# Performance work log

Measured on AMD Instinct MI355X. Metric: run time of the kernel, lower is better.

Reference implementation:

```python
import jax, jax.numpy as jnp
import numpy as np

N_EMBEDDING = 512
EMBEDDING_DIM = 64
COMMITMENT_COST = 0.25


def setup_inputs() -> dict:
    key = jax.random.key(0)
    k1, k2 = jax.random.split(key)
    inputs = jax.random.normal(k1, (64, 32, 32, EMBEDDING_DIM), dtype=jnp.float32)
    context = jnp.zeros((1,), dtype=jnp.float32)  # unused by the module
    # variance_scaling(1.0, 'fan_in', 'uniform') on shape (D, K): fan_in = D
    limit = np.sqrt(3.0 / EMBEDDING_DIM)
    embeddings = jax.random.uniform(
        k2, (EMBEDDING_DIM, N_EMBEDDING), dtype=jnp.float32,
        minval=-limit, maxval=limit)
    return {"inputs": inputs, "context": context, "embeddings": embeddings}


def reference(inputs, context, embeddings):
    D, K = embeddings.shape
    flat = inputs.reshape(-1, D)  # [N, D]
    distances = (
        jnp.sum(jnp.square(flat), axis=1, keepdims=True)
        - 2.0 * jnp.matmul(flat, embeddings)
        + jnp.sum(jnp.square(embeddings), axis=0, keepdims=True)
    )
    encoding_indices_flat = jnp.argmax(-distances, axis=1)  # [N]
    encodings = jax.nn.one_hot(encoding_indices_flat, K, dtype=distances.dtype)
    encoding_indices = encoding_indices_flat.reshape(inputs.shape[:-1])
    # gather codebook rows: embeddings.T is [K, D]
    quantized = embeddings.T[encoding_indices]  # [B, H, W, D]

    e_latent_loss = jnp.mean(jnp.square(jax.lax.stop_gradient(quantized) - inputs))
    q_latent_loss = jnp.mean(jnp.square(quantized - jax.lax.stop_gradient(inputs)))
    loss = q_latent_loss + COMMITMENT_COST * e_latent_loss

    # straight-through estimator
    quantized = inputs + jax.lax.stop_gradient(quantized - inputs)

    avg_probs = jnp.mean(encodings, axis=0)
    perplexity = jnp.exp(-jnp.sum(avg_probs * jnp.log(avg_probs + 1e-10)))
    return (quantized, loss, perplexity, encodings, encoding_indices, distances)
```

## Files before the change

### kernel.cpp

```cpp
#include <hip/hip_runtime.h>


#define NROWS 65536
#define DIM 64
#define KCODES 512
#define ROWS_PER_BLOCK 64
#define NBLOCKS (NROWS / ROWS_PER_BLOCK)
#define RPW 8

#define QUANT_OFF 0ull
#define LOSS_OFF  4194304ull
#define PERP_OFF  4194305ull
#define ENC_OFF   4194306ull
#define IDX_OFF   37748738ull
#define DIST_OFF  37814274ull

typedef float f32x4 __attribute__((ext_vector_type(4)));

__global__ __launch_bounds__(64) void vq_transpose(
    const float* __restrict__ emb, float* __restrict__ et)
{
    const int t = blockIdx.x * 64 + threadIdx.x;
    f32x4* et4 = (f32x4*)et;
#pragma unroll
    for (int dq = 0; dq < 16; ++dq) {
        f32x4 v;
        v.x = emb[(dq * 4 + 0) * KCODES + t];
        v.y = emb[(dq * 4 + 1) * KCODES + t];
        v.z = emb[(dq * 4 + 2) * KCODES + t];
        v.w = emb[(dq * 4 + 3) * KCODES + t];
        et4[t * 16 + dq] = v;
    }
}

__global__ __launch_bounds__(512, 2) void vq_main(
    const float* __restrict__ inp, const float* __restrict__ emb,
    const float* __restrict__ et,
    float* __restrict__ out, int* __restrict__ hist,
    float* __restrict__ loss_part)
{
    __shared__ f32x4 s_E[16 * KCODES];
    __shared__ f32x4 s_X[ROWS_PER_BLOCK * 16];
    __shared__ float s_sumx2[ROWS_PER_BLOCK];
    __shared__ float s_loss[8];

    const int tid  = threadIdx.x;
    const int w    = tid >> 6;
    const int lane = tid & 63;
    const int rbase = blockIdx.x * ROWS_PER_BLOCK;
    const int rl0  = w * RPW;

    {
        const f32x4* e4 = (const f32x4*)emb;
#pragma unroll
        for (int i = 0; i < 16; ++i)
            s_E[i * 512 + tid] = e4[i * 512 + tid];
    }
    {
        const f32x4* inp4 = (const f32x4*)inp + (size_t)blockIdx.x * 1024;
        s_X[tid]       = inp4[tid];
        s_X[512 + tid] = inp4[512 + tid];
    }
    __syncthreads();

    {
        const int row_l = w * RPW + (lane >> 3);
        const int q = lane & 7;
        const f32x4 a = s_X[row_l * 16 + q * 2 + 0];
        const f32x4 b = s_X[row_l * 16 + q * 2 + 1];
        float p = 0.f;
        p = fmaf(a.x, a.x, p); p = fmaf(a.y, a.y, p);
        p = fmaf(a.z, a.z, p); p = fmaf(a.w, a.w, p);
        p = fmaf(b.x, b.x, p); p = fmaf(b.y, b.y, p);
        p = fmaf(b.z, b.z, p); p = fmaf(b.w, b.w, p);
        p += __shfl_xor(p, 1);
        p += __shfl_xor(p, 2);
        p += __shfl_xor(p, 4);
        if (q == 0) s_sumx2[row_l] = p;
    }

    f32x4 sume2_0 = {0.f, 0.f, 0.f, 0.f};
    f32x4 sume2_1 = {0.f, 0.f, 0.f, 0.f};
    float loss_acc = 0.f;

    f32x4 acc[RPW][2];
#pragma unroll
    for (int r = 0; r < RPW; ++r) {
        acc[r][0] = (f32x4){0.f, 0.f, 0.f, 0.f};
        acc[r][1] = (f32x4){0.f, 0.f, 0.f, 0.f};
    }

#pragma unroll 1
    for (int dq = 0; dq < 16; ++dq) {
        f32x4 e0[4], e1[4];
#pragma unroll
        for (int sub = 0; sub < 4; ++sub) {
            e0[sub] = s_E[(dq * 4 + sub) * 128 + lane];
            e1[sub] = s_E[(dq * 4 + sub) * 128 + 64 + lane];
        }
#pragma unroll
        for (int sub = 0; sub < 4; ++sub) {
            sume2_0 = sume2_0 + e0[sub] * e0[sub];
            sume2_1 = sume2_1 + e1[sub] * e1[sub];
        }
#pragma unroll
        for (int r = 0; r < RPW; ++r) {
            const f32x4 xv = s_X[(rl0 + r) * 16 + dq];
            acc[r][0] = acc[r][0] + xv.x * e0[0];
            acc[r][1] = acc[r][1] + xv.x * e1[0];
            acc[r][0] = acc[r][0] + xv.y * e0[1];
            acc[r][1] = acc[r][1] + xv.y * e1[1];
            acc[r][0] = acc[r][0] + xv.z * e0[2];
            acc[r][1] = acc[r][1] + xv.z * e1[2];
            acc[r][0] = acc[r][0] + xv.w * e0[3];
            acc[r][1] = acc[r][1] + xv.w * e1[3];
        }
    }

    const f32x4* et4 = (const f32x4*)et;

#pragma unroll
    for (int r = 0; r < RPW; ++r) {
        const int row = rbase + rl0 + r;
        const float sx2 = s_sumx2[rl0 + r];

        const f32x4 dd0 = (sume2_0 + sx2) + (-2.f) * acc[r][0];
        const f32x4 dd1 = (sume2_1 + sx2) + (-2.f) * acc[r][1];

        f32x4* dp = (f32x4*)(out + DIST_OFF) + (size_t)row * 128;
        __builtin_nontemporal_store(dd0, dp + lane);
        __builtin_nontemporal_store(dd1, dp + 64 + lane);

        float bd = fminf(fminf(fminf(dd0.x, dd0.y), fminf(dd0.z, dd0.w)),
                         fminf(fminf(dd1.x, dd1.y), fminf(dd1.z, dd1.w)));
        const int kb = lane * 4;
        int ck = 0x7fffffff;
        if (dd1.w == bd) ck = 256 + kb + 3;
        if (dd1.z == bd) ck = 256 + kb + 2;
        if (dd1.y == bd) ck = 256 + kb + 1;
        if (dd1.x == bd) ck = 256 + kb + 0;
        if (dd0.w == bd) ck = kb + 3;
        if (dd0.z == bd) ck = kb + 2;
        if (dd0.y == bd) ck = kb + 1;
        if (dd0.x == bd) ck = kb + 0;

        float fd = bd;
#pragma unroll
        for (int off = 32; off; off >>= 1)
            fd = fminf(fd, __shfl_xor(fd, off));
        int c2 = (bd == fd) ? ck : 0x7fffffff;
#pragma unroll
        for (int off = 32; off; off >>= 1) {
            const int ok = __shfl_xor(c2, off);
            c2 = ok < c2 ? ok : c2;
        }

        f32x4* ep = (f32x4*)(out + ENC_OFF) + (size_t)row * 128;
        const int cq = c2 >> 2;
        f32x4 v0 = {0.f, 0.f, 0.f, 0.f};
        f32x4 v1 = {0.f, 0.f, 0.f, 0.f};
        if (cq == lane) {
            v0.x = (c2 & 3) == 0 ? 1.f : 0.f;
            v0.y = (c2 & 3) == 1 ? 1.f : 0.f;
            v0.z = (c2 & 3) == 2 ? 1.f : 0.f;
            v0.w = (c2 & 3) == 3 ? 1.f : 0.f;
        }
        if (cq == 64 + lane) {
            v1.x = (c2 & 3) == 0 ? 1.f : 0.f;
            v1.y = (c2 & 3) == 1 ? 1.f : 0.f;
            v1.z = (c2 & 3) == 2 ? 1.f : 0.f;
            v1.w = (c2 & 3) == 3 ? 1.f : 0.f;
        }
        __builtin_nontemporal_store(v0, ep + lane);
        __builtin_nontemporal_store(v1, ep + 64 + lane);

        if (lane < 16) {
            const f32x4 q = et4[c2 * 16 + lane];
            ((f32x4*)(out + QUANT_OFF + (size_t)row * DIM))[lane] = q;
        }

        if (lane == 0) {
            out[IDX_OFF + row] = (float)c2;
            atomicAdd(&hist[c2], 1);
            loss_acc += fd;
        }
    }

    if (lane == 0) s_loss[w] = loss_acc;
    __syncthreads();
    if (tid == 0) {
        float s = 0.f;
#pragma unroll
        for (int i = 0; i < 8; ++i) s += s_loss[i];
        loss_part[blockIdx.x] = s;
    }
}

__global__ __launch_bounds__(512) void vq_final(
    const int* __restrict__ hist, const float* __restrict__ loss_part,
    float* __restrict__ out)
{
    __shared__ float s_red[8];
    __shared__ float s_red2[8];
    const int tid = threadIdx.x;
    const int w = tid >> 6, lane = tid & 63;

    float p = (float)hist[tid] * (1.f / 65536.f);
    float t = p * logf(p + 1e-10f);
    float l = loss_part[tid] + loss_part[tid + 512];
#pragma unroll
    for (int off = 32; off; off >>= 1) {
        t += __shfl_xor(t, off);
        l += __shfl_xor(l, off);
    }
    if (lane == 0) { s_red[w] = t; s_red2[w] = l; }
    __syncthreads();
    if (tid == 0) {
        float s = 0.f, ls = 0.f;
#pragma unroll
        for (int i = 0; i < 8; ++i) { s += s_red[i]; ls += s_red2[i]; }
        out[PERP_OFF] = expf(-s);
        out[LOSS_OFF] = ls * (1.25f / 4194304.f);
    }
}

extern "C" void kernel_launch(void* const* d_in, const int* in_sizes, int n_in,
                              void* d_out, int out_size, void* d_ws, size_t ws_size,
                              hipStream_t stream) {
    const float* inp = (const float*)d_in[0];
    const float* emb = (const float*)d_in[2];
    float* out = (float*)d_out;
    int*   hist      = (int*)d_ws;
    float* loss_part = (float*)((char*)d_ws + 2048);
    float* et        = (float*)((char*)d_ws + 8192);

    (void)hipMemsetAsync(d_ws, 0, 2048, stream);
    vq_transpose<<<dim3(8), dim3(64), 0, stream>>>(emb, et);
    vq_main<<<dim3(NBLOCKS), dim3(512), 0, stream>>>(
        inp, emb, et, out, hist, loss_part);
    vq_final<<<dim3(1), dim3(512), 0, stream>>>(hist, loss_part, out);
}
```

Before: 112.6 us.

## Drop shared-memory codebook, read embeddings from cache, batch epilogue stores

Removes the 128KB LDS codebook copy per block and loads codebook vectors directly from global memory in the inner loop, raising launch bounds to four blocks per CU. The epilogue is split so all argmin reductions and quantized-row gathers happen first, then all output stores are issued together. This aims to increase occupancy and cut per-block LDS fill cost, at the risk of slower cached global loads in the distance loop and higher register pressure from holding distances and gathered rows.

```diff
diff --git a/kernel.cpp b/kernel.cpp
--- a/kernel.cpp
+++ b/kernel.cpp
@@ -33,13 +33,12 @@
     }
 }
 
-__global__ __launch_bounds__(512, 2) void vq_main(
+__global__ __launch_bounds__(512, 4) void vq_main(
     const float* __restrict__ inp, const float* __restrict__ emb,
     const float* __restrict__ et,
     float* __restrict__ out, int* __restrict__ hist,
     float* __restrict__ loss_part)
 {
-    __shared__ f32x4 s_E[16 * KCODES];
     __shared__ f32x4 s_X[ROWS_PER_BLOCK * 16];
     __shared__ float s_sumx2[ROWS_PER_BLOCK];
     __shared__ float s_loss[8];
@@ -50,12 +49,6 @@
     const int rbase = blockIdx.x * ROWS_PER_BLOCK;
     const int rl0  = w * RPW;
 
-    {
-        const f32x4* e4 = (const f32x4*)emb;
-#pragma unroll
-        for (int i = 0; i < 16; ++i)
-            s_E[i * 512 + tid] = e4[i * 512 + tid];
-    }
     {
         const f32x4* inp4 = (const f32x4*)inp + (size_t)blockIdx.x * 1024;
         s_X[tid]       = inp4[tid];
@@ -90,13 +83,15 @@
         acc[r][1] = (f32x4){0.f, 0.f, 0.f, 0.f};
     }
 
+    const float* ebase = emb + lane * 4;
+
 #pragma unroll 1
     for (int dq = 0; dq < 16; ++dq) {
         f32x4 e0[4], e1[4];
 #pragma unroll
         for (int sub = 0; sub < 4; ++sub) {
-            e0[sub] = s_E[(dq * 4 + sub) * 128 + lane];
-            e1[sub] = s_E[(dq * 4 + sub) * 128 + 64 + lane];
+            e0[sub] = *(const f32x4*)(ebase + (dq * 4 + sub) * KCODES);
+            e1[sub] = *(const f32x4*)(ebase + (dq * 4 + sub) * KCODES + 256);
         }
 #pragma unroll
         for (int sub = 0; sub < 4; ++sub) {
@@ -119,17 +114,15 @@
 
     const f32x4* et4 = (const f32x4*)et;
 
+    int   c2a[RPW];
+    f32x4 qv[RPW];
 #pragma unroll
     for (int r = 0; r < RPW; ++r) {
-        const int row = rbase + rl0 + r;
         const float sx2 = s_sumx2[rl0 + r];
-
         const f32x4 dd0 = (sume2_0 + sx2) + (-2.f) * acc[r][0];
         const f32x4 dd1 = (sume2_1 + sx2) + (-2.f) * acc[r][1];
-
-        f32x4* dp = (f32x4*)(out + DIST_OFF) + (size_t)row * 128;
-        __builtin_nontemporal_store(dd0, dp + lane);
-        __builtin_nontemporal_store(dd1, dp + 64 + lane);
+        acc[r][0] = dd0;
+        acc[r][1] = dd1;
 
         float bd = fminf(fminf(fminf(dd0.x, dd0.y), fminf(dd0.z, dd0.w)),
                          fminf(fminf(dd1.x, dd1.y), fminf(dd1.z, dd1.w)));
@@ -154,6 +147,20 @@
             const int ok = __shfl_xor(c2, off);
             c2 = ok < c2 ? ok : c2;
         }
+        c2a[r] = c2;
+        if (lane == 0) loss_acc += fd;
+
+        if (lane < 16) qv[r] = et4[c2 * 16 + lane];
+    }
+
+#pragma unroll
+    for (int r = 0; r < RPW; ++r) {
+        const int row = rbase + rl0 + r;
+        const int c2 = c2a[r];
+
+        f32x4* dp = (f32x4*)(out + DIST_OFF) + (size_t)row * 128;
+        __builtin_nontemporal_store(acc[r][0], dp + lane);
+        __builtin_nontemporal_store(acc[r][1], dp + 64 + lane);
 
         f32x4* ep = (f32x4*)(out + ENC_OFF) + (size_t)row * 128;
         const int cq = c2 >> 2;
@@ -174,15 +181,12 @@
         __builtin_nontemporal_store(v0, ep + lane);
         __builtin_nontemporal_store(v1, ep + 64 + lane);
 
-        if (lane < 16) {
-            const f32x4 q = et4[c2 * 16 + lane];
-            ((f32x4*)(out + QUANT_OFF + (size_t)row * DIM))[lane] = q;
-        }
+        if (lane < 16)
+            ((f32x4*)(out + QUANT_OFF + (size_t)row * DIM))[lane] = qv[r];
 
         if (lane == 0) {
             out[IDX_OFF + row] = (float)c2;
             atomicAdd(&hist[c2], 1);
-            loss_acc += fd;
         }
     }
 
```

Result: faster. 107.7 us (-4.4%).

## Drop shared codebook, stream embeddings from global in two half passes

Applied to the files above, without the earlier changes.

Removes the 128KB shared-memory codebook copy and has each wave read embedding columns directly from global/L2 in two 256-code passes. Accumulators per row drop by half and launch bounds go up to 4 blocks per CU for higher occupancy. A running argmin is merged across passes, and each pass writes its distance half and zeroes its one-hot half immediately. Afterwards only the single one-hot lane is rewritten, which depends on the ordering of the two stores to the same address. The pass order is staggered by wave and block to spread global access.

```diff
diff --git a/kernel.cpp b/kernel.cpp
--- a/kernel.cpp
+++ b/kernel.cpp
@@ -33,13 +33,12 @@
     }
 }
 
-__global__ __launch_bounds__(512, 2) void vq_main(
+__global__ __launch_bounds__(512, 4) void vq_main(
     const float* __restrict__ inp, const float* __restrict__ emb,
     const float* __restrict__ et,
     float* __restrict__ out, int* __restrict__ hist,
     float* __restrict__ loss_part)
 {
-    __shared__ f32x4 s_E[16 * KCODES];
     __shared__ f32x4 s_X[ROWS_PER_BLOCK * 16];
     __shared__ float s_sumx2[ROWS_PER_BLOCK];
     __shared__ float s_loss[8];
@@ -50,12 +49,6 @@
     const int rbase = blockIdx.x * ROWS_PER_BLOCK;
     const int rl0  = w * RPW;
 
-    {
-        const f32x4* e4 = (const f32x4*)emb;
-#pragma unroll
-        for (int i = 0; i < 16; ++i)
-            s_E[i * 512 + tid] = e4[i * 512 + tid];
-    }
     {
         const f32x4* inp4 = (const f32x4*)inp + (size_t)blockIdx.x * 1024;
         s_X[tid]       = inp4[tid];
@@ -79,42 +72,72 @@
         if (q == 0) s_sumx2[row_l] = p;
     }
 
-    f32x4 sume2_0 = {0.f, 0.f, 0.f, 0.f};
-    f32x4 sume2_1 = {0.f, 0.f, 0.f, 0.f};
+    float bd[RPW];
+    int   ck[RPW];
+#pragma unroll
+    for (int r = 0; r < RPW; ++r) { bd[r] = 3.4e38f; ck[r] = 0x7fffffff; }
+
+    const float* ebase = emb + lane * 4;
     float loss_acc = 0.f;
 
-    f32x4 acc[RPW][2];
-#pragma unroll
-    for (int r = 0; r < RPW; ++r) {
-        acc[r][0] = (f32x4){0.f, 0.f, 0.f, 0.f};
-        acc[r][1] = (f32x4){0.f, 0.f, 0.f, 0.f};
-    }
+    auto pass = [&](auto hc) {
+        constexpr int H = decltype(hc)::value;
+        f32x4 acc[RPW];
+#pragma unroll
+        for (int r = 0; r < RPW; ++r) acc[r] = (f32x4){0.f, 0.f, 0.f, 0.f};
+        f32x4 se = {0.f, 0.f, 0.f, 0.f};
 
 #pragma unroll 1
-    for (int dq = 0; dq < 16; ++dq) {
-        f32x4 e0[4], e1[4];
-#pragma unroll
-        for (int sub = 0; sub < 4; ++sub) {
-            e0[sub] = s_E[(dq * 4 + sub) * 128 + lane];
-            e1[sub] = s_E[(dq * 4 + sub) * 128 + 64 + lane];
-        }
-#pragma unroll
-        for (int sub = 0; sub < 4; ++sub) {
-            sume2_0 = sume2_0 + e0[sub] * e0[sub];
-            sume2_1 = sume2_1 + e1[sub] * e1[sub];
-        }
+        for (int dq = 0; dq < 16; ++dq) {
+            f32x4 e4[4];
+#pragma unroll
+            for (int sub = 0; sub < 4; ++sub)
+                e4[sub] = *(const f32x4*)(ebase + (dq * 4 + sub) * KCODES
+                                          + H * 256);
+#pragma unroll
+            for (int sub = 0; sub < 4; ++sub)
+                se = se + e4[sub] * e4[sub];
+#pragma unroll
+            for (int r = 0; r < RPW; ++r) {
+                const f32x4 xv = s_X[(rl0 + r) * 16 + dq];
+                acc[r] = acc[r] + xv.x * e4[0];
+                acc[r] = acc[r] + xv.y * e4[1];
+                acc[r] = acc[r] + xv.z * e4[2];
+                acc[r] = acc[r] + xv.w * e4[3];
+            }
+        }
+
+        const f32x4 zero = {0.f, 0.f, 0.f, 0.f};
 #pragma unroll
         for (int r = 0; r < RPW; ++r) {
-            const f32x4 xv = s_X[(rl0 + r) * 16 + dq];
-            acc[r][0] = acc[r][0] + xv.x * e0[0];
-            acc[r][1] = acc[r][1] + xv.x * e1[0];
-            acc[r][0] = acc[r][0] + xv.y * e0[1];
-            acc[r][1] = acc[r][1] + xv.y * e1[1];
-            acc[r][0] = acc[r][0] + xv.z * e0[2];
-            acc[r][1] = acc[r][1] + xv.z * e1[2];
-            acc[r][0] = acc[r][0] + xv.w * e0[3];
-            acc[r][1] = acc[r][1] + xv.w * e1[3];
-        }
+            const int row = rbase + rl0 + r;
+            const f32x4 dd = (se + s_sumx2[rl0 + r]) + (-2.f) * acc[r];
+
+            f32x4* dp = (f32x4*)(out + DIST_OFF) + (size_t)row * 128;
+            __builtin_nontemporal_store(dd, dp + H * 64 + lane);
+            f32x4* ep = (f32x4*)(out + ENC_OFF) + (size_t)row * 128;
+            __builtin_nontemporal_store(zero, ep + H * 64 + lane);
+
+            const float m = fminf(fminf(dd.x, dd.y), fminf(dd.z, dd.w));
+            int j = 3;
+            if (dd.z == m) j = 2;
+            if (dd.y == m) j = 1;
+            if (dd.x == m) j = 0;
+            const int kk = H * 256 + lane * 4 + j;
+            if (m < bd[r] || (m == bd[r] && kk < ck[r])) {
+                bd[r] = m;
+                ck[r] = kk;
+            }
+        }
+    };
+
+    const int first = ((w >> 2) ^ blockIdx.x) & 1;
+    if (first == 0) {
+        pass(std::integral_constant<int, 0>{});
+        pass(std::integral_constant<int, 1>{});
+    } else {
+        pass(std::integral_constant<int, 1>{});
+        pass(std::integral_constant<int, 0>{});
     }
 
     const f32x4* et4 = (const f32x4*)et;
@@ -122,57 +145,28 @@
 #pragma unroll
     for (int r = 0; r < RPW; ++r) {
         const int row = rbase + rl0 + r;
-        const float sx2 = s_sumx2[rl0 + r];
-
-        const f32x4 dd0 = (sume2_0 + sx2) + (-2.f) * acc[r][0];
-        const f32x4 dd1 = (sume2_1 + sx2) + (-2.f) * acc[r][1];
-
-        f32x4* dp = (f32x4*)(out + DIST_OFF) + (size_t)row * 128;
-        __builtin_nontemporal_store(dd0, dp + lane);
-        __builtin_nontemporal_store(dd1, dp + 64 + lane);
-
-        float bd = fminf(fminf(fminf(dd0.x, dd0.y), fminf(dd0.z, dd0.w)),
-                         fminf(fminf(dd1.x, dd1.y), fminf(dd1.z, dd1.w)));
-        const int kb = lane * 4;
-        int ck = 0x7fffffff;
-        if (dd1.w == bd) ck = 256 + kb + 3;
-        if (dd1.z == bd) ck = 256 + kb + 2;
-        if (dd1.y == bd) ck = 256 + kb + 1;
-        if (dd1.x == bd) ck = 256 + kb + 0;
-        if (dd0.w == bd) ck = kb + 3;
-        if (dd0.z == bd) ck = kb + 2;
-        if (dd0.y == bd) ck = kb + 1;
-        if (dd0.x == bd) ck = kb + 0;
-
-        float fd = bd;
+
+        float fd = bd[r];
 #pragma unroll
         for (int off = 32; off; off >>= 1)
             fd = fminf(fd, __shfl_xor(fd, off));
-        int c2 = (bd == fd) ? ck : 0x7fffffff;
+        int c2 = (bd[r] == fd) ? ck[r] : 0x7fffffff;
 #pragma unroll
         for (int off = 32; off; off >>= 1) {
             const int ok = __shfl_xor(c2, off);
             c2 = ok < c2 ? ok : c2;
         }
 
-        f32x4* ep = (f32x4*)(out + ENC_OFF) + (size_t)row * 128;
-        const int cq = c2 >> 2;
-        f32x4 v0 = {0.f, 0.f, 0.f, 0.f};
-        f32x4 v1 = {0.f, 0.f, 0.f, 0.f};
-        if (cq == lane) {
-            v0.x = (c2 & 3) == 0 ? 1.f : 0.f;
-            v0.y = (c2 & 3) == 1 ? 1.f : 0.f;
-            v0.z = (c2 & 3) == 2 ? 1.f : 0.f;
-            v0.w = (c2 & 3) == 3 ? 1.f : 0.f;
-        }
-        if (cq == 64 + lane) {
-            v1.x = (c2 & 3) == 0 ? 1.f : 0.f;
-            v1.y = (c2 & 3) == 1 ? 1.f : 0.f;
-            v1.z = (c2 & 3) == 2 ? 1.f : 0.f;
-            v1.w = (c2 & 3) == 3 ? 1.f : 0.f;
-        }
-        __builtin_nontemporal_store(v0, ep + lane);
-        __builtin_nontemporal_store(v1, ep + 64 + lane);
+        const int slot = c2 >> 2;
+        if (lane == (slot & 63)) {
+            f32x4 v;
+            v.x = (c2 & 3) == 0 ? 1.f : 0.f;
+            v.y = (c2 & 3) == 1 ? 1.f : 0.f;
+            v.z = (c2 & 3) == 2 ? 1.f : 0.f;
+            v.w = (c2 & 3) == 3 ? 1.f : 0.f;
+            f32x4* ep = (f32x4*)(out + ENC_OFF) + (size_t)row * 128;
+            __builtin_nontemporal_store(v, ep + slot);
+        }
 
         if (lane < 16) {
             const f32x4 q = et4[c2 * 16 + lane];
```

New measurement: 114.3 us. Within noise of the previous version (+1.5%).
